# Optimization experiments

Measured on AMD Instinct MI355X. Metric: run time of the kernel, lower is better.

The kernel has to match this reference:

```python
import jax, jax.numpy as jnp
import numpy as np

B, N, D = 4, 4096, 256

def setup_inputs() -> dict:
    key = jax.random.key(0)
    ks = jax.random.split(key, 7)
    def xavier(k, shape):
        fan_in, fan_out = shape[1], shape[0]
        a = jnp.sqrt(6.0 / (fan_in + fan_out))
        return jax.random.uniform(k, shape, jnp.float32, -a, a)
    return {
        "x": jax.random.normal(ks[0], (B, N, D), jnp.float32),
        "Wq": xavier(ks[1], (D, D)),
        "bq": jnp.zeros((D,), jnp.float32),
        "Wk": xavier(ks[2], (D, D)),
        "bk": jnp.zeros((D,), jnp.float32),
        "Wv": xavier(ks[3], (D, D)),
        "bv": jnp.zeros((D,), jnp.float32),
        "scale": jnp.asarray([jnp.sqrt(jnp.float32(D))]),
    }

def reference(x, Wq, bq, Wk, bk, Wv, bv, scale):
    # nn.Linear: y = x @ W.T + b
    q = jnp.einsum('bnd,ed->bne', x, Wq) + bq
    k = jnp.einsum('bnd,ed->bne', x, Wk) + bk
    v = jnp.einsum('bnd,ed->bne', x, Wv) + bv
    scores = jnp.einsum('bqd,bkd->bqk', q, k) / scale[0]  # [B,N,N]
    attn = jax.nn.softmax(scores, axis=-1)
    out = jnp.einsum('bqk,bkd->bqd', attn, v)
    return out
```

## Files before the change

### kernel.cpp

```cpp
#include <hip/hip_runtime.h>
#include <hip/hip_bf16.h>

typedef unsigned int u32;
typedef unsigned short u16;
typedef __attribute__((ext_vector_type(8))) __bf16 bf8v;
typedef __attribute__((ext_vector_type(16))) float f32x16;
typedef __attribute__((ext_vector_type(8))) u16 u16x8;

__device__ inline u16 f2bf(float f) {
    u32 u = __float_as_uint(f);
    u = (u + 0x7FFF + ((u >> 16) & 1)) >> 16;
    return (u16)u;
}
__device__ inline u32 pk2(float a, float b) {
    return (u32)f2bf(a) | ((u32)f2bf(b) << 16);
}
__device__ inline float bf2f(u16 h) { return __uint_as_float(((u32)h) << 16); }

__device__ inline u32 cvtpk(float a, float b) {
    u32 r;
    asm("v_cvt_pk_bf16_f32 %0, %1, %2" : "=v"(r) : "v"(a), "v"(b));
    return r;
}
__device__ inline void plswap(u32& a, u32& b) {
    asm("v_permlane32_swap_b32 %0, %1" : "+v"(a), "+v"(b));
}

__device__ inline void dma16(const u16* g, u16* l) {
    __builtin_amdgcn_global_load_lds(
        (const __attribute__((address_space(1))) void*)g,
        (__attribute__((address_space(3))) void*)l, 16, 0, 0);
}

__global__ void cvt_all(const float* __restrict__ x,
                        const float* __restrict__ wq, const float* __restrict__ wk,
                        const float* __restrict__ wv,
                        u16* __restrict__ xp, u16* __restrict__ wall) {
    const int blk = blockIdx.x;
    if (blk < 2048) {
        int g = blk * 256 + threadIdx.x;
        int row = g >> 5, cp = g & 31;
        const float* s = x + row * 256 + cp * 8;
        float4 a = *(const float4*)s;
        float4 b = *(const float4*)(s + 4);
        uint4 o;
        o.x = pk2(a.x, a.y); o.y = pk2(a.z, a.w);
        o.z = pk2(b.x, b.y); o.w = pk2(b.z, b.w);
        *(uint4*)(xp + (row >> 5) * 8192 + cp * 256 + (row & 31) * 8) = o;
    } else {
        const int bb = blk - 2048;
        const int m = bb >> 5;
        const float* src = m == 0 ? wq : m == 1 ? wk : wv;
        int g = (bb & 31) * 256 + threadIdx.x;
        int row = g >> 5, c = g & 31;
        const float* s = src + row * 256 + c * 8;
        float4 a = *(const float4*)s;
        float4 b = *(const float4*)(s + 4);
        uint4 o;
        o.x = pk2(a.x, a.y); o.y = pk2(a.z, a.w);
        o.z = pk2(b.x, b.y); o.w = pk2(b.z, b.w);
        *(uint4*)(wall + m * 65536 + row * 256 + ((c ^ (row & 7)) * 8)) = o;
    }
}

__global__ __launch_bounds__(256) void qkv_proj(
    const u16* __restrict__ xp, const u16* __restrict__ wall,
    const float* __restrict__ bq, const float* __restrict__ bk, const float* __restrict__ bv,
    u16* __restrict__ qp, u16* __restrict__ kp, u16* __restrict__ vp)
{
    __shared__ u16 Ws[64 * 256];

    const int blk = blockIdx.x;
    const int xcd = blk & 7;
    const int s2 = blk >> 3;
    const int rt = s2 / 12;
    const int yz = s2 % 12;
    const int sel = yz >> 2;
    const int colbase = (yz & 3) * 64;
    const int rowbase0 = (xcd * 16 + rt) * 128;

    const float* bias = sel == 0 ? bq : sel == 1 ? bk : bv;
    const int tid = threadIdx.x;
    const int wave = tid >> 6, lane = tid & 63;
    const int l31 = lane & 31, l5 = lane >> 5;
    const int tg = (rowbase0 >> 5) + wave;

    {
        const u16* wsrc = wall + sel * 65536 + colbase * 256;
#pragma unroll
        for (int j = 0; j < 8; j++) {
            const int i = wave * 8 + j;
            dma16(wsrc + i * 512 + lane * 8, Ws + i * 512);
        }
    }
    asm volatile("s_waitcnt vmcnt(0)" ::: "memory");
    __syncthreads();

    f32x16 acc0, acc1;
#pragma unroll
    for (int j = 0; j < 16; j++) { acc0[j] = 0.f; acc1[j] = 0.f; }

    const u16* ap = xp + tg * 8192 + l5 * 256 + l31 * 8;
    const int sw = l31 & 7;
#pragma unroll
    for (int kk = 0; kk < 16; kk++) {
        bf8v af = *(const bf8v*)(ap + kk * 512);
        bf8v b0 = *(const bf8v*)(Ws + l31 * 256 + (((kk * 2 + l5) ^ sw) * 8));
        bf8v b1 = *(const bf8v*)(Ws + (32 + l31) * 256 + (((kk * 2 + l5) ^ sw) * 8));
        acc0 = __builtin_amdgcn_mfma_f32_32x32x16_bf16(af, b0, acc0, 0, 0, 0);
        acc1 = __builtin_amdgcn_mfma_f32_32x32x16_bf16(af, b1, acc1, 0, 0, 0);
    }

    const float bias0 = bias[colbase + l31], bias1 = bias[colbase + 32 + l31];
    if (sel < 2) {
        u16* base = (sel == 0 ? qp : kp) + tg * 8192;
        const int c0 = (colbase >> 3) + (l31 >> 3), j0 = l31 & 7;
#pragma unroll
        for (int r = 0; r < 16; r++) {
            const int R = (r & 3) + 8 * (r >> 2) + 4 * l5;
            base[c0 * 256 + R * 8 + j0]       = f2bf(acc0[r] + bias0);
            base[(c0 + 4) * 256 + R * 8 + j0] = f2bf(acc1[r] + bias1);
        }
    } else {
        u16* base = vp + tg * 8192;
        const int d0 = colbase + l31, d1 = d0 + 32;
#pragma unroll
        for (int r = 0; r < 16; r++) {
            const int R = (r & 3) + 8 * (r >> 2) + 4 * l5;
            base[(R >> 3) * 2048 + d0 * 8 + (R & 7)] = f2bf(acc0[r] + bias0);
            base[(R >> 3) * 2048 + d1 * 8 + (R & 7)] = f2bf(acc1[r] + bias1);
        }
    }
}

__global__ __launch_bounds__(256, 2) void flash_attn(
    const u16* __restrict__ qp_, const u16* __restrict__ kp_, const u16* __restrict__ vp_,
    const float* __restrict__ scale,
    u16* __restrict__ Opb, float* __restrict__ ml)
{
    __shared__ u16 Ks[2 * 8192];
    __shared__ u16 Vs[2 * 8192];

    const int tid = threadIdx.x;
    const int wave = tid >> 6, lane = tid & 63;
    const int l31 = lane & 31, l5 = lane >> 5;

    const int blk = blockIdx.x;
    const int slot = blk >> 3;
    const int g = (blk & 7) * 2 + (slot >> 5);
    const int qtile = slot & 31;
    const int b = g >> 2, s = g & 3;
    const int qbase = qtile * 128 + wave * 32;
    const float is2 = 1.44269504088896f / scale[0];

    union { u16x8 u; bf8v v; } oneu;
#pragma unroll
    for (int j = 0; j < 8; j++) oneu.u[j] = 0x3F80;
    const bf8v ones = oneu.v;

    bf8v qf[16];
    {
        const u16* qp = qp_ + (b * 128 + qtile * 4 + wave) * 8192 + l31 * 8;
#pragma unroll
        for (int kk = 0; kk < 16; kk++)
            qf[kk] = *(const bf8v*)(qp + (kk * 2 + l5) * 256);
    }

    f32x16 o[8];
#pragma unroll
    for (int i = 0; i < 8; i++)
#pragma unroll
        for (int j = 0; j < 16; j++) o[i][j] = 0.f;
    f32x16 ls;
#pragma unroll
    for (int j = 0; j < 16; j++) ls[j] = 0.f;

    const u16* kbase = kp_ + (b * 128 + s * 32) * 8192;
    const u16* vbase = vp_ + (b * 128 + s * 32) * 8192;

#pragma unroll
    for (int j = 0; j < 4; j++) {
        const int i = wave * 4 + j;
        dma16(kbase + i * 512 + lane * 8, Ks + i * 512);
    }
#pragma unroll
    for (int j = 0; j < 4; j++) {
        const int i = wave * 4 + j;
        dma16(vbase + i * 512 + lane * 8, Vs + i * 512);
    }
#pragma unroll
    for (int j = 0; j < 4; j++) {
        const int i = wave * 4 + j;
        dma16(kbase + 8192 + i * 512 + lane * 8, Ks + 8192 + i * 512);
    }
    asm volatile("s_waitcnt vmcnt(8)" ::: "memory");
    asm volatile("s_barrier" ::: "memory");

    bf8v pf0, pf1;
    {
        f32x16 c0, c1;
#pragma unroll
        for (int j = 0; j < 16; j++) { c0[j] = 0.f; c1[j] = 0.f; }
#pragma unroll
        for (int j = 0; j < 8; j++) {
            bf8v kf0 = *(const bf8v*)(Ks + (j * 2 + l5) * 256 + l31 * 8);
            c0 = __builtin_amdgcn_mfma_f32_32x32x16_bf16(kf0, qf[j], c0, 0, 0, 0);
            bf8v kf1 = *(const bf8v*)(Ks + ((8 + j) * 2 + l5) * 256 + l31 * 8);
            c1 = __builtin_amdgcn_mfma_f32_32x32x16_bf16(kf1, qf[8 + j], c1, 0, 0, 0);
        }
        float e[16];
#pragma unroll
        for (int r = 0; r < 16; r++)
            e[r] = __builtin_amdgcn_exp2f((c0[r] + c1[r]) * is2);
        u32 pA = cvtpk(e[0], e[1]), pB = cvtpk(e[2], e[3]);
        u32 pC = cvtpk(e[4], e[5]), pD = cvtpk(e[6], e[7]);
        plswap(pA, pC); plswap(pB, pD);
        u32 pE = cvtpk(e[8], e[9]),  pF = cvtpk(e[10], e[11]);
        u32 pG = cvtpk(e[12], e[13]), pH = cvtpk(e[14], e[15]);
        plswap(pE, pG); plswap(pF, pH);
        union { uint4 u; bf8v v; } u0, u1;
        u0.u = (uint4){pA, pB, pC, pD};
        u1.u = (uint4){pE, pF, pG, pH};
        pf0 = u0.v; pf1 = u1.v;
    }

#pragma unroll 1
    for (int it = 0; it < 31; it++) {
        const int buf = it & 1;
        asm volatile("s_waitcnt vmcnt(0)" ::: "memory");
        asm volatile("s_barrier" ::: "memory");
        {
            const u16* vt_ = vbase + (it + 1) * 8192;
#pragma unroll
            for (int j = 0; j < 4; j++) {
                const int i = wave * 4 + j;
                dma16(vt_ + i * 512 + lane * 8, Vs + (buf ^ 1) * 8192 + i * 512);
            }
            if (it < 30) {
                const u16* kt_ = kbase + (it + 2) * 8192;
#pragma unroll
                for (int j = 0; j < 4; j++) {
                    const int i = wave * 4 + j;
                    dma16(kt_ + i * 512 + lane * 8, Ks + buf * 8192 + i * 512);
                }
            }
        }
        const u16* Kb_ = Ks + (buf ^ 1) * 8192;
        f32x16 c0, c1;
#pragma unroll
        for (int j = 0; j < 16; j++) { c0[j] = 0.f; c1[j] = 0.f; }
#pragma unroll
        for (int j = 0; j < 8; j++) {
            bf8v kf0 = *(const bf8v*)(Kb_ + (j * 2 + l5) * 256 + l31 * 8);
            c0 = __builtin_amdgcn_mfma_f32_32x32x16_bf16(kf0, qf[j], c0, 0, 0, 0);
            bf8v kf1 = *(const bf8v*)(Kb_ + ((8 + j) * 2 + l5) * 256 + l31 * 8);
            c1 = __builtin_amdgcn_mfma_f32_32x32x16_bf16(kf1, qf[8 + j], c1, 0, 0, 0);
        }
        const u16* Vb_ = Vs + buf * 8192;
        ls = __builtin_amdgcn_mfma_f32_32x32x16_bf16(pf0, ones, ls, 0, 0, 0);
        ls = __builtin_amdgcn_mfma_f32_32x32x16_bf16(pf1, ones, ls, 0, 0, 0);
        float e[16];
#pragma unroll
        for (int j = 0; j < 8; j++) {
            bf8v vf0 = *(const bf8v*)(Vb_ + (l5 * 256 + j * 32 + l31) * 8);
            o[j] = __builtin_amdgcn_mfma_f32_32x32x16_bf16(pf0, vf0, o[j], 0, 0, 0);
            e[2 * j] = __builtin_amdgcn_exp2f((c0[2 * j] + c1[2 * j]) * is2);
            bf8v vf1 = *(const bf8v*)(Vb_ + ((2 + l5) * 256 + j * 32 + l31) * 8);
            o[j] = __builtin_amdgcn_mfma_f32_32x32x16_bf16(pf1, vf1, o[j], 0, 0, 0);
            e[2 * j + 1] = __builtin_amdgcn_exp2f((c0[2 * j + 1] + c1[2 * j + 1]) * is2);
        }
        {
            u32 pA = cvtpk(e[0], e[1]), pB = cvtpk(e[2], e[3]);
            u32 pC = cvtpk(e[4], e[5]), pD = cvtpk(e[6], e[7]);
            plswap(pA, pC); plswap(pB, pD);
            u32 pE = cvtpk(e[8], e[9]),  pF = cvtpk(e[10], e[11]);
            u32 pG = cvtpk(e[12], e[13]), pH = cvtpk(e[14], e[15]);
            plswap(pE, pG); plswap(pF, pH);
            union { uint4 u; bf8v v; } u0, u1;
            u0.u = (uint4){pA, pB, pC, pD};
            u1.u = (uint4){pE, pF, pG, pH};
            pf0 = u0.v; pf1 = u1.v;
        }
    }

    asm volatile("s_waitcnt vmcnt(0)" ::: "memory");
    asm volatile("s_barrier" ::: "memory");
    {
        const u16* Vb_ = Vs + 8192;
        ls = __builtin_amdgcn_mfma_f32_32x32x16_bf16(pf0, ones, ls, 0, 0, 0);
        ls = __builtin_amdgcn_mfma_f32_32x32x16_bf16(pf1, ones, ls, 0, 0, 0);
#pragma unroll
        for (int j = 0; j < 8; j++) {
            bf8v vf0 = *(const bf8v*)(Vb_ + (l5 * 256 + j * 32 + l31) * 8);
            o[j] = __builtin_amdgcn_mfma_f32_32x32x16_bf16(pf0, vf0, o[j], 0, 0, 0);
            bf8v vf1 = *(const bf8v*)(Vb_ + ((2 + l5) * 256 + j * 32 + l31) * 8);
            o[j] = __builtin_amdgcn_mfma_f32_32x32x16_bf16(pf1, vf1, o[j], 0, 0, 0);
        }
    }

    const int rowg = s * 16384 + b * 4096 + qbase;
    u16* ob = Opb + (size_t)rowg * 256;
#pragma unroll
    for (int nb = 0; nb < 8; nb++)
#pragma unroll
        for (int r = 0; r < 16; r++) {
            const int R = (r & 3) + 8 * (r >> 2) + 4 * l5;
            ob[R * 256 + nb * 32 + l31] = f2bf(o[nb][r]);
        }
    if (l31 == 0)
#pragma unroll
        for (int r = 0; r < 16; r++) {
            const int R = (r & 3) + 8 * (r >> 2) + 4 * l5;
            ml[rowg + R] = ls[r];
        }
}

__global__ __launch_bounds__(256) void combine(
    const u16* __restrict__ Opb, const float* __restrict__ ml, float* __restrict__ out)
{
    const int row = blockIdx.x * 4 + (threadIdx.x >> 6);
    const int lane = threadIdx.x & 63;
    const float denom = ml[row] + ml[16384 + row] + ml[32768 + row] + ml[49152 + row];
    float4 acc = {0.f, 0.f, 0.f, 0.f};
#pragma unroll
    for (int si = 0; si < 4; si++) {
        ushort4 v = *(const ushort4*)(Opb + ((size_t)si * 16384 + row) * 256 + lane * 4);
        acc.x += bf2f(v.x); acc.y += bf2f(v.y);
        acc.z += bf2f(v.z); acc.w += bf2f(v.w);
    }
    const float inv = 1.0f / denom;
    acc.x *= inv; acc.y *= inv; acc.z *= inv; acc.w *= inv;
    *((float4*)(out + (size_t)row * 256) + lane) = acc;
}

extern "C" void kernel_launch(void* const* d_in, const int* in_sizes, int n_in,
                              void* d_out, int out_size, void* d_ws, size_t ws_size,
                              hipStream_t stream) {
    const float* x     = (const float*)d_in[0];
    const float* Wq    = (const float*)d_in[1];
    const float* bq    = (const float*)d_in[2];
    const float* Wk    = (const float*)d_in[3];
    const float* bk    = (const float*)d_in[4];
    const float* Wv    = (const float*)d_in[5];
    const float* bv    = (const float*)d_in[6];
    const float* scale = (const float*)d_in[7];
    float* out = (float*)d_out;

    char* ws = (char*)d_ws;
    u16* xp   = (u16*)ws;
    u16* qp   = (u16*)(ws + (8u  << 20));
    u16* kp   = (u16*)(ws + (16u << 20));
    u16* vp   = (u16*)(ws + (24u << 20));
    u16* wall = (u16*)(ws + (32u << 20));
    u16* Opb  = (u16*)(ws + (34u << 20));
    float* ml = (float*)(ws + (66u << 20));

    cvt_all<<<2144, 256, 0, stream>>>(x, Wq, Wk, Wv, xp, wall);
    qkv_proj<<<1536, 256, 0, stream>>>(xp, wall, bq, bk, bv, qp, kp, vp);
    flash_attn<<<512, 256, 0, stream>>>(qp, kp, vp, scale, Opb, ml);
    combine<<<4096, 256, 0, stream>>>(Opb, ml, out);
}
```

Before: 182.8 us.

## Fold softmax scale into Q projection and widen QKV tiles to 128 columns

```diff
diff --git a/kernel.cpp b/kernel.cpp
--- a/kernel.cpp
+++ b/kernel.cpp
@@ -66,20 +66,22 @@
 __global__ __launch_bounds__(256) void qkv_proj(
     const u16* __restrict__ xp, const u16* __restrict__ wall,
     const float* __restrict__ bq, const float* __restrict__ bk, const float* __restrict__ bv,
+    const float* __restrict__ scale,
     u16* __restrict__ qp, u16* __restrict__ kp, u16* __restrict__ vp)
 {
-    __shared__ u16 Ws[64 * 256];
+    __shared__ u16 Ws[128 * 256];
 
     const int blk = blockIdx.x;
     const int xcd = blk & 7;
-    const int s2 = blk >> 3;
-    const int rt = s2 / 12;
-    const int yz = s2 % 12;
-    const int sel = yz >> 2;
-    const int colbase = (yz & 3) * 64;
+    const int r2 = blk >> 3;
+    const int rt = r2 / 6;
+    const int cz = r2 % 6;
+    const int sel = cz >> 1;
+    const int colbase = (cz & 1) * 128;
     const int rowbase0 = (xcd * 16 + rt) * 128;
 
     const float* bias = sel == 0 ? bq : sel == 1 ? bk : bv;
+    const float qs = sel == 0 ? 1.44269504088896f / scale[0] : 1.0f;
     const int tid = threadIdx.x;
     const int wave = tid >> 6, lane = tid & 63;
     const int l31 = lane & 31, l5 = lane >> 5;
@@ -88,54 +90,64 @@
     {
         const u16* wsrc = wall + sel * 65536 + colbase * 256;
 #pragma unroll
-        for (int j = 0; j < 8; j++) {
-            const int i = wave * 8 + j;
+        for (int j = 0; j < 16; j++) {
+            const int i = wave * 16 + j;
             dma16(wsrc + i * 512 + lane * 8, Ws + i * 512);
         }
     }
     asm volatile("s_waitcnt vmcnt(0)" ::: "memory");
     __syncthreads();
 
-    f32x16 acc0, acc1;
-#pragma unroll
-    for (int j = 0; j < 16; j++) { acc0[j] = 0.f; acc1[j] = 0.f; }
+    f32x16 acc[4];
+#pragma unroll
+    for (int cb = 0; cb < 4; cb++)
+#pragma unroll
+        for (int j = 0; j < 16; j++) acc[cb][j] = 0.f;
 
     const u16* ap = xp + tg * 8192 + l5 * 256 + l31 * 8;
     const int sw = l31 & 7;
 #pragma unroll
     for (int kk = 0; kk < 16; kk++) {
         bf8v af = *(const bf8v*)(ap + kk * 512);
-        bf8v b0 = *(const bf8v*)(Ws + l31 * 256 + (((kk * 2 + l5) ^ sw) * 8));
-        bf8v b1 = *(const bf8v*)(Ws + (32 + l31) * 256 + (((kk * 2 + l5) ^ sw) * 8));
-        acc0 = __builtin_amdgcn_mfma_f32_32x32x16_bf16(af, b0, acc0, 0, 0, 0);
-        acc1 = __builtin_amdgcn_mfma_f32_32x32x16_bf16(af, b1, acc1, 0, 0, 0);
-    }
-
-    const float bias0 = bias[colbase + l31], bias1 = bias[colbase + 32 + l31];
+        const int co = ((kk * 2 + l5) ^ sw) * 8;
+#pragma unroll
+        for (int cb = 0; cb < 4; cb++) {
+            bf8v bfr = *(const bf8v*)(Ws + (cb * 32 + l31) * 256 + co);
+            acc[cb] = __builtin_amdgcn_mfma_f32_32x32x16_bf16(af, bfr, acc[cb], 0, 0, 0);
+        }
+    }
+
     if (sel < 2) {
         u16* base = (sel == 0 ? qp : kp) + tg * 8192;
-        const int c0 = (colbase >> 3) + (l31 >> 3), j0 = l31 & 7;
-#pragma unroll
-        for (int r = 0; r < 16; r++) {
-            const int R = (r & 3) + 8 * (r >> 2) + 4 * l5;
-            base[c0 * 256 + R * 8 + j0]       = f2bf(acc0[r] + bias0);
-            base[(c0 + 4) * 256 + R * 8 + j0] = f2bf(acc1[r] + bias1);
+#pragma unroll
+        for (int cb = 0; cb < 4; cb++) {
+            const int colb = colbase + cb * 32;
+            const float bc = bias[colb + l31];
+            const int c0 = (colb >> 3) + (l31 >> 3), j0 = l31 & 7;
+#pragma unroll
+            for (int r = 0; r < 16; r++) {
+                const int R = (r & 3) + 8 * (r >> 2) + 4 * l5;
+                base[c0 * 256 + R * 8 + j0] = f2bf((acc[cb][r] + bc) * qs);
+            }
         }
     } else {
         u16* base = vp + tg * 8192;
-        const int d0 = colbase + l31, d1 = d0 + 32;
-#pragma unroll
-        for (int r = 0; r < 16; r++) {
-            const int R = (r & 3) + 8 * (r >> 2) + 4 * l5;
-            base[(R >> 3) * 2048 + d0 * 8 + (R & 7)] = f2bf(acc0[r] + bias0);
-            base[(R >> 3) * 2048 + d1 * 8 + (R & 7)] = f2bf(acc1[r] + bias1);
+#pragma unroll
+        for (int cb = 0; cb < 4; cb++) {
+            const int colb = colbase + cb * 32;
+            const float bc = bias[colb + l31];
+            const int d0 = colb + l31;
+#pragma unroll
+            for (int r = 0; r < 16; r++) {
+                const int R = (r & 3) + 8 * (r >> 2) + 4 * l5;
+                base[(R >> 3) * 2048 + d0 * 8 + (R & 7)] = f2bf(acc[cb][r] + bc);
+            }
         }
     }
 }
 
 __global__ __launch_bounds__(256, 2) void flash_attn(
     const u16* __restrict__ qp_, const u16* __restrict__ kp_, const u16* __restrict__ vp_,
-    const float* __restrict__ scale,
     u16* __restrict__ Opb, float* __restrict__ ml)
 {
     __shared__ u16 Ks[2 * 8192];
@@ -151,7 +163,6 @@
     const int qtile = slot & 31;
     const int b = g >> 2, s = g & 3;
     const int qbase = qtile * 128 + wave * 32;
-    const float is2 = 1.44269504088896f / scale[0];
 
     union { u16x8 u; bf8v v; } oneu;
 #pragma unroll
@@ -211,7 +222,7 @@
         float e[16];
 #pragma unroll
         for (int r = 0; r < 16; r++)
-            e[r] = __builtin_amdgcn_exp2f((c0[r] + c1[r]) * is2);
+            e[r] = __builtin_amdgcn_exp2f(c0[r] + c1[r]);
         u32 pA = cvtpk(e[0], e[1]), pB = cvtpk(e[2], e[3]);
         u32 pC = cvtpk(e[4], e[5]), pD = cvtpk(e[6], e[7]);
         plswap(pA, pC); plswap(pB, pD);
@@ -264,10 +275,10 @@
         for (int j = 0; j < 8; j++) {
             bf8v vf0 = *(const bf8v*)(Vb_ + (l5 * 256 + j * 32 + l31) * 8);
             o[j] = __builtin_amdgcn_mfma_f32_32x32x16_bf16(pf0, vf0, o[j], 0, 0, 0);
-            e[2 * j] = __builtin_amdgcn_exp2f((c0[2 * j] + c1[2 * j]) * is2);
+            e[2 * j] = __builtin_amdgcn_exp2f(c0[2 * j] + c1[2 * j]);
             bf8v vf1 = *(const bf8v*)(Vb_ + ((2 + l5) * 256 + j * 32 + l31) * 8);
             o[j] = __builtin_amdgcn_mfma_f32_32x32x16_bf16(pf1, vf1, o[j], 0, 0, 0);
-            e[2 * j + 1] = __builtin_amdgcn_exp2f((c0[2 * j + 1] + c1[2 * j + 1]) * is2);
+            e[2 * j + 1] = __builtin_amdgcn_exp2f(c0[2 * j + 1] + c1[2 * j + 1]);
         }
         {
             u32 pA = cvtpk(e[0], e[1]), pB = cvtpk(e[2], e[3]);
@@ -356,7 +367,7 @@
     float* ml = (float*)(ws + (66u << 20));
 
     cvt_all<<<2144, 256, 0, stream>>>(x, Wq, Wk, Wv, xp, wall);
-    qkv_proj<<<1536, 256, 0, stream>>>(xp, wall, bq, bk, bv, qp, kp, vp);
-    flash_attn<<<512, 256, 0, stream>>>(qp, kp, vp, scale, Opb, ml);
+    qkv_proj<<<768, 256, 0, stream>>>(xp, wall, bq, bk, bv, scale, qp, kp, vp);
+    flash_attn<<<512, 256, 0, stream>>>(qp, kp, vp, Opb, ml);
     combine<<<4096, 256, 0, stream>>>(Opb, ml, out);
 }
```

Measured after the change: 178.0 us. 1.03x faster.
